# Kernel optimization log

Hardware: AMD Instinct MI355X
Metric: run time of the kernel (lower is better)

The kernel has to match this reference:

```python
import jax, jax.numpy as jnp
import numpy as np

B, S, H, NH, E, F = 4, 1024, 1024, 16, 8, 4096
D = H // NH  # head_dim = 64
EPS = 1e-5


def _layernorm(x, g, b):
    mu = jnp.mean(x, axis=-1, keepdims=True)
    var = jnp.var(x, axis=-1, keepdims=True)
    return (x - mu) * jax.lax.rsqrt(var + EPS) * g + b


def setup_inputs() -> dict:
    key = jax.random.key(0)
    ks = jax.random.split(key, 16)
    s = 0.02
    return {
        "x": jax.random.normal(ks[0], (B, S, H), jnp.float32),
        "ln1_g": jnp.ones((H,), jnp.float32),
        "ln1_b": jnp.zeros((H,), jnp.float32),
        "ln2_g": jnp.ones((H,), jnp.float32),
        "ln2_b": jnp.zeros((H,), jnp.float32),
        "wq": jax.random.normal(ks[1], (H, H), jnp.float32) * s,
        "bq": jnp.zeros((H,), jnp.float32),
        "wk": jax.random.normal(ks[2], (H, H), jnp.float32) * s,
        "bk": jnp.zeros((H,), jnp.float32),
        "wv": jax.random.normal(ks[3], (H, H), jnp.float32) * s,
        "bv": jnp.zeros((H,), jnp.float32),
        "wo": jax.random.normal(ks[4], (H, H), jnp.float32) * s,
        "bo": jnp.zeros((H,), jnp.float32),
        "gate_w": jax.random.normal(ks[5], (H, E), jnp.float32) * s,
        "gate_b": jnp.zeros((E,), jnp.float32),
        "w1": jax.random.normal(ks[6], (E, H, F), jnp.float32) * s,
        "b1": jnp.zeros((E, F), jnp.float32),
        "w2": jax.random.normal(ks[7], (E, F, H), jnp.float32) * s,
        "b2": jnp.zeros((E, H), jnp.float32),
    }


def reference(x, ln1_g, ln1_b, ln2_g, ln2_b, wq, bq, wk, bk, wv, bv, wo, bo,
              gate_w, gate_b, w1, b1, w2, b2):
    b, s, h = x.shape
    # ---- attention sub-layer ----
    hn = _layernorm(x, ln1_g, ln1_b)
    q = (hn @ wq + bq).reshape(b, s, NH, D).transpose(0, 2, 1, 3)  # [B,NH,S,D]
    k = (hn @ wk + bk).reshape(b, s, NH, D).transpose(0, 2, 1, 3)
    v = (hn @ wv + bv).reshape(b, s, NH, D).transpose(0, 2, 1, 3)
    scores = jnp.einsum('bhqd,bhkd->bhqk', q, k) / jnp.sqrt(jnp.float32(D))
    attn = jax.nn.softmax(scores, axis=-1)
    o = jnp.einsum('bhqk,bhkd->bhqd', attn, v)
    o = o.transpose(0, 2, 1, 3).reshape(b, s, h)
    x = x + (o @ wo + bo)
    # ---- MoE sub-layer (top-1 routing; output NOT scaled by gate prob) ----
    hn2 = _layernorm(x, ln2_g, ln2_b).reshape(-1, h)  # [T,H]
    logits = hn2 @ gate_w + gate_b                    # [T,E]
    idx = jnp.argmax(logits, axis=-1)                 # argmax(softmax)=argmax(logits)
    # dense compute of all experts, then top-1 select (jit-friendly dispatch)
    mid = jax.nn.relu(jnp.einsum('th,ehf->etf', hn2, w1) + b1[:, None, :])  # [E,T,F]
    y = jnp.einsum('etf,efh->eth', mid, w2) + b2[:, None, :]                # [E,T,H]
    moe = y[idx, jnp.arange(hn2.shape[0])]            # [T,H]
    return x + moe.reshape(b, s, h)
```

## Files before the change

### kernel.cpp

```cpp
#include <hip/hip_runtime.h>
#include <math.h>


constexpr int NB = 4, NS = 1024, NHID = 1024, NHEAD = 16, HD = 64, NE = 8, NF = 4096;
constexpr int NT = NB * NS;
constexpr float LN_EPS = 1e-5f;
constexpr size_t MiB = 1048576;

using bf16x8 = __attribute__((ext_vector_type(8))) short;
using f32x4  = __attribute__((ext_vector_type(4))) float;
using f32x16 = __attribute__((ext_vector_type(16))) float;
using u32x2  = __attribute__((ext_vector_type(2))) unsigned int;

__device__ __forceinline__ unsigned short f2bf(float x) {
    unsigned u = __float_as_uint(x);
    return (unsigned short)((u + 0x7fffu + ((u >> 16) & 1u)) >> 16);
}
__device__ __forceinline__ float bf2f(unsigned short h) {
    return __uint_as_float((unsigned)h << 16);
}

__device__ __forceinline__ void gload_lds16(const void* g, void* l) {
    __builtin_amdgcn_global_load_lds(
        (const __attribute__((address_space(1))) void*)g,
        (__attribute__((address_space(3))) void*)l, 16, 0, 0);
}

template<int MODE>
__global__ __launch_bounds__(256)
void ln_kernel(const float* __restrict__ x, const float* __restrict__ g,
               const float* __restrict__ b, float* __restrict__ y,
               unsigned short* __restrict__ yh, unsigned short* __restrict__ yl)
{
    const int t = blockIdx.x, tid = threadIdx.x;
    const float4 xv = ((const float4*)(x + (size_t)t * NHID))[tid];
    float s  = xv.x + xv.y + xv.z + xv.w;
    float sq = xv.x*xv.x + xv.y*xv.y + xv.z*xv.z + xv.w*xv.w;
    for (int off = 32; off > 0; off >>= 1) {
        s  += __shfl_down(s, off);
        sq += __shfl_down(sq, off);
    }
    __shared__ float ws_[4], wsq_[4], stats[2];
    const int wid = tid >> 6, lane = tid & 63;
    if (lane == 0) { ws_[wid] = s; wsq_[wid] = sq; }
    __syncthreads();
    if (tid == 0) {
        const float ts = ws_[0] + ws_[1] + ws_[2] + ws_[3];
        const float tq = wsq_[0] + wsq_[1] + wsq_[2] + wsq_[3];
        const float mu = ts * (1.0f / NHID);
        const float var = tq * (1.0f / NHID) - mu * mu;
        stats[0] = mu; stats[1] = rsqrtf(var + LN_EPS);
    }
    __syncthreads();
    const float mu = stats[0], rs = stats[1];
    const float4 gv = ((const float4*)g)[tid];
    const float4 bv = ((const float4*)b)[tid];
    float ov[4];
    ov[0] = (xv.x - mu) * rs * gv.x + bv.x;
    ov[1] = (xv.y - mu) * rs * gv.y + bv.y;
    ov[2] = (xv.z - mu) * rs * gv.z + bv.z;
    ov[3] = (xv.w - mu) * rs * gv.w + bv.w;
    if (MODE == 1) {
        float4 o4; o4.x = ov[0]; o4.y = ov[1]; o4.z = ov[2]; o4.w = ov[3];
        ((float4*)(y + (size_t)t * NHID))[tid] = o4;
    }
    unsigned long long ph = 0, pl = 0;
    #pragma unroll
    for (int j = 0; j < 4; ++j) {
        const unsigned short h = f2bf(ov[j]);
        ph |= (unsigned long long)h << (16 * j);
        if (MODE == 0) pl |= (unsigned long long)f2bf(ov[j] - bf2f(h)) << (16 * j);
    }
    ((unsigned long long*)(yh + (size_t)t * NHID))[tid] = ph;
    if (MODE == 0)
        ((unsigned long long*)(yl + (size_t)t * NHID))[tid] = pl;
}

__global__ __launch_bounds__(256)
void pack_whl(const float* __restrict__ w, unsigned short* __restrict__ out,
              int K, int N)
{
    const int k8 = blockIdx.y;
    const int col = blockIdx.x * 256 + threadIdx.x;
    const float* src = w + (size_t)k8 * 8 * N + col;
    unsigned short th[8] __attribute__((aligned(16)));
    unsigned short tl[8] __attribute__((aligned(16)));
    #pragma unroll
    for (int j = 0; j < 8; ++j) {
        const float f = src[(size_t)j * N];
        th[j] = f2bf(f);
        tl[j] = f2bf(f - bf2f(th[j]));
    }
    const size_t plane = (size_t)(K / 8) * N * 8;
    const size_t o = ((size_t)k8 * N + col) * 8;
    *(f32x4*)(out + o)         = *(const f32x4*)th;
    *(f32x4*)(out + plane + o) = *(const f32x4*)tl;
}

__global__ __launch_bounds__(256)
void pack_w(const float* __restrict__ w, unsigned short* __restrict__ out,
            int K, int N)
{
    const int e = blockIdx.z, k8 = blockIdx.y;
    const int col = blockIdx.x * 256 + threadIdx.x;
    const float* src = w + ((size_t)e * K + (size_t)k8 * 8) * N + col;
    unsigned short tmp[8] __attribute__((aligned(16)));
    #pragma unroll
    for (int j = 0; j < 8; ++j) tmp[j] = f2bf(src[(size_t)j * N]);
    *(f32x4*)(out + (((size_t)e * (K / 8) + k8) * N + col) * 8) = *(const f32x4*)tmp;
}

template<bool QKV3, bool RESID>
__global__ __launch_bounds__(256, 2)
void gemm3(const unsigned short* __restrict__ Ah, const unsigned short* __restrict__ Al,
           const unsigned short* __restrict__ Bp,
           const float* __restrict__ b0, const float* __restrict__ b1,
           const float* __restrict__ b2,
           const float* __restrict__ resid, float* __restrict__ C,
           int N, int K)
{
    __shared__ __attribute__((aligned(16))) unsigned short Ahs[4 * 128 * 8];
    __shared__ __attribute__((aligned(16))) unsigned short Als[4 * 128 * 8];
    __shared__ __attribute__((aligned(16))) unsigned short Bhs[4 * 128 * 8];
    __shared__ __attribute__((aligned(16))) unsigned short Bls[4 * 128 * 8];

    const int z  = QKV3 ? blockIdx.z : 0;
    const int m0 = blockIdx.y * 128;
    const int n0 = blockIdx.x * 128;
    const size_t plane = (size_t)(K / 8) * N * 8;
    const unsigned short* Bh = Bp + (size_t)z * 2 * plane;
    const unsigned short* Bl = Bh + plane;
    const float* bp = QKV3 ? (z == 0 ? b0 : z == 1 ? b1 : b2) : b0;
    float* Cp = C + (QKV3 ? (size_t)z * NT * N : 0);

    const int tid  = threadIdx.x;
    const int lane = tid & 63, wid = tid >> 6;
    const int quad = lane >> 4, l16 = lane & 15;
    const int wm = (wid >> 1) * 64;
    const int wn = (wid & 1) * 64;

    const unsigned short *gAh[2], *gAl[2], *gBh[2], *gBl[2];
    void *lAh[2], *lAl[2], *lBh[2], *lBl[2];
    #pragma unroll
    for (int i = 0; i < 2; ++i) {
        const int c = tid + 256 * i;
        const int q = c >> 7, idx = c & 127;
        gAh[i] = Ah + (size_t)(m0 + idx) * K + q * 8;
        gAl[i] = Al + (size_t)(m0 + idx) * K + q * 8;
        gBh[i] = Bh + ((size_t)q * N + n0 + idx) * 8;
        gBl[i] = Bl + ((size_t)q * N + n0 + idx) * 8;
        lAh[i] = (void*)&Ahs[(size_t)c * 8];
        lAl[i] = (void*)&Als[(size_t)c * 8];
        lBh[i] = (void*)&Bhs[(size_t)c * 8];
        lBl[i] = (void*)&Bls[(size_t)c * 8];
    }

    f32x4 acc[4][4];
    #pragma unroll
    for (int mi = 0; mi < 4; ++mi)
        #pragma unroll
        for (int ni = 0; ni < 4; ++ni)
            acc[mi][ni] = (f32x4){0.f, 0.f, 0.f, 0.f};

    const size_t bstep = (size_t)4 * N * 8;
    for (int ks = 0; ks < K / 32; ++ks) {
        __syncthreads();
        #pragma unroll
        for (int i = 0; i < 2; ++i) {
            gload_lds16(gAh[i], lAh[i]);
            gload_lds16(gAl[i], lAl[i]);
            gload_lds16(gBh[i], lBh[i]);
            gload_lds16(gBl[i], lBl[i]);
            gAh[i] += 32; gAl[i] += 32; gBh[i] += bstep; gBl[i] += bstep;
        }
        __syncthreads();

        bf16x8 ah[4], al[4], bh[4], bl[4];
        #pragma unroll
        for (int mi = 0; mi < 4; ++mi) {
            ah[mi] = *(const bf16x8*)&Ahs[((size_t)quad * 128 + wm + mi * 16 + l16) * 8];
            al[mi] = *(const bf16x8*)&Als[((size_t)quad * 128 + wm + mi * 16 + l16) * 8];
        }
        #pragma unroll
        for (int ni = 0; ni < 4; ++ni) {
            bh[ni] = *(const bf16x8*)&Bhs[((size_t)quad * 128 + wn + ni * 16 + l16) * 8];
            bl[ni] = *(const bf16x8*)&Bls[((size_t)quad * 128 + wn + ni * 16 + l16) * 8];
        }
        #pragma unroll
        for (int mi = 0; mi < 4; ++mi)
            #pragma unroll
            for (int ni = 0; ni < 4; ++ni) {
                acc[mi][ni] = __builtin_amdgcn_mfma_f32_16x16x32_bf16(
                    ah[mi], bh[ni], acc[mi][ni], 0, 0, 0);
                acc[mi][ni] = __builtin_amdgcn_mfma_f32_16x16x32_bf16(
                    ah[mi], bl[ni], acc[mi][ni], 0, 0, 0);
                acc[mi][ni] = __builtin_amdgcn_mfma_f32_16x16x32_bf16(
                    al[mi], bh[ni], acc[mi][ni], 0, 0, 0);
            }
    }

    #pragma unroll
    for (int mi = 0; mi < 4; ++mi) {
        const int rbase = wm + mi * 16 + quad * 4;
        #pragma unroll
        for (int r = 0; r < 4; ++r) {
            const size_t gm = m0 + rbase + r;
            #pragma unroll
            for (int ni = 0; ni < 4; ++ni) {
                const int col = n0 + wn + ni * 16 + l16;
                float vv = acc[mi][ni][r] + bp[col];
                if (RESID) vv += resid[gm * N + col];
                Cp[gm * N + col] = vv;
            }
        }
    }
}

__global__ __launch_bounds__(256, 2)
void attn_kernel(const float* __restrict__ q, const float* __restrict__ k,
                 const float* __restrict__ v,
                 unsigned short* __restrict__ oh, unsigned short* __restrict__ ol)
{
    struct KV {
        unsigned short Kp[2][4160];
        unsigned short Vp[2][4096];
    };
    __shared__ union SMem { KV kv; float O[4 * 64 * 33]; } sm;
    __shared__ float linv[128];

    const int qt = blockIdx.x, hh = blockIdx.y, b = blockIdx.z;
    const int tid = threadIdx.x;
    const int lane = tid & 63, w = tid >> 6;
    const int l31 = lane & 31, hf = lane >> 5;

    const size_t rowbase = (size_t)b * NS;
    const size_t cb = (size_t)hh * HD;

    float4 kreg[4], vreg[2][2];
    auto loadKV = [&](int kt) {
        #pragma unroll
        for (int i = 0; i < 4; ++i) {
            const int c = tid + 256 * i, j = c >> 4, d4 = (c & 15) << 2;
            kreg[i] = *(const float4*)(k + (rowbase + kt * 64 + j) * NHID + cb + d4);
        }
        #pragma unroll
        for (int i = 0; i < 2; ++i) {
            const int c = tid + 256 * i;
            const int j2 = ((c >> 6) << 3) + (((c >> 4) & 3) << 1);
            const int d4 = (c & 15) << 2;
            vreg[i][0] = *(const float4*)(v + (rowbase + kt * 64 + j2) * NHID + cb + d4);
            vreg[i][1] = *(const float4*)(v + (rowbase + kt * 64 + j2 + 1) * NHID + cb + d4);
        }
    };
    loadKV(0);

    bf16x8 qfh[4], qfl[4];
    {
        const int qrow = qt * 128 + w * 32 + l31;
        const float* qp = q + (rowbase + qrow) * NHID + cb + hf * 8;
        #pragma unroll
        for (int s = 0; s < 4; ++s) {
            const float4 f0 = *(const float4*)(qp + s * 16);
            const float4 f1 = *(const float4*)(qp + s * 16 + 4);
            const float ff[8] = {f0.x, f0.y, f0.z, f0.w, f1.x, f1.y, f1.z, f1.w};
            #pragma unroll
            for (int e = 0; e < 8; ++e) {
                const float sv = ff[e] * 0.125f;
                const unsigned short hv = f2bf(sv);
                qfh[s][e] = (short)hv;
                qfl[s][e] = (short)f2bf(sv - bf2f(hv));
            }
        }
    }

    f32x16 oa[2];
    #pragma unroll
    for (int mfd = 0; mfd < 2; ++mfd)
        #pragma unroll
        for (int r = 0; r < 16; ++r) oa[mfd][r] = 0.f;
    float m_run = -1e30f, l_run = 0.f;

    for (int kt = 0; kt < NS / 64; ++kt) {
        __syncthreads();

        #pragma unroll
        for (int i = 0; i < 4; ++i) {
            const int c = tid + 256 * i, j = c >> 4, d4 = (c & 15) << 2;
            const float* f = (const float*)&kreg[i];
            unsigned short hs[4], ls[4];
            #pragma unroll
            for (int e = 0; e < 4; ++e) {
                hs[e] = f2bf(f[e]); ls[e] = f2bf(f[e] - bf2f(hs[e]));
            }
            u32x2 wh, wl;
            wh[0] = hs[0] | ((unsigned)hs[1] << 16); wh[1] = hs[2] | ((unsigned)hs[3] << 16);
            wl[0] = ls[0] | ((unsigned)ls[1] << 16); wl[1] = ls[2] | ((unsigned)ls[3] << 16);
            const int ad = (d4 >> 3) * 520 + j * 8 + (d4 & 7);
            *(u32x2*)&sm.kv.Kp[0][ad] = wh;
            *(u32x2*)&sm.kv.Kp[1][ad] = wl;
        }
        #pragma unroll
        for (int i = 0; i < 2; ++i) {
            const int c = tid + 256 * i;
            const int j2 = ((c >> 6) << 3) + (((c >> 4) & 3) << 1);
            const int d4 = (c & 15) << 2;
            const float* fa = (const float*)&vreg[i][0];
            const float* fb = (const float*)&vreg[i][1];
            #pragma unroll
            for (int dd = 0; dd < 4; ++dd) {
                const int d = d4 + dd;
                const unsigned short ah_ = f2bf(fa[dd]), bh_ = f2bf(fb[dd]);
                const unsigned short al_ = f2bf(fa[dd] - bf2f(ah_));
                const unsigned short bl_ = f2bf(fb[dd] - bf2f(bh_));
                const int ad = d * 64 + (((j2 >> 3) ^ (d & 7)) << 3) + (j2 & 7);
                *(unsigned*)&sm.kv.Vp[0][ad] = ah_ | ((unsigned)bh_ << 16);
                *(unsigned*)&sm.kv.Vp[1][ad] = al_ | ((unsigned)bl_ << 16);
            }
        }
        if (kt + 1 < NS / 64) loadKV(kt + 1);
        __syncthreads();

        f32x16 sa[2];
        #pragma unroll
        for (int mf = 0; mf < 2; ++mf)
            #pragma unroll
            for (int r = 0; r < 16; ++r) sa[mf][r] = 0.f;
        #pragma unroll
        for (int mf = 0; mf < 2; ++mf) {
            bf16x8 kf[4];
            #pragma unroll
            for (int s = 0; s < 4; ++s)
                kf[s] = *(const bf16x8*)&sm.kv.Kp[0][(2*s+hf)*520 + (mf*32+l31)*8];
            #pragma unroll
            for (int s = 0; s < 4; ++s)
                sa[mf] = __builtin_amdgcn_mfma_f32_32x32x16_bf16(kf[s], qfh[s], sa[mf], 0, 0, 0);
            #pragma unroll
            for (int s = 0; s < 4; ++s)
                sa[mf] = __builtin_amdgcn_mfma_f32_32x32x16_bf16(kf[s], qfl[s], sa[mf], 0, 0, 0);
            #pragma unroll
            for (int s = 0; s < 4; ++s)
                kf[s] = *(const bf16x8*)&sm.kv.Kp[1][(2*s+hf)*520 + (mf*32+l31)*8];
            #pragma unroll
            for (int s = 0; s < 4; ++s)
                sa[mf] = __builtin_amdgcn_mfma_f32_32x32x16_bf16(kf[s], qfh[s], sa[mf], 0, 0, 0);
        }

        float tm = sa[0][0];
        #pragma unroll
        for (int r = 1; r < 16; ++r) tm = fmaxf(tm, sa[0][r]);
        #pragma unroll
        for (int r = 0; r < 16; ++r) tm = fmaxf(tm, sa[1][r]);
        tm = fmaxf(tm, __shfl_xor(tm, 32));
        const float newm = fmaxf(m_run, tm);
        const float al = __expf(m_run - newm);
        m_run = newm;
        float ps = 0.f;
        #pragma unroll
        for (int mf = 0; mf < 2; ++mf)
            #pragma unroll
            for (int r = 0; r < 16; ++r) {
                const float pv = __expf(sa[mf][r] - newm);
                sa[mf][r] = pv; ps += pv;
            }
        ps += __shfl_xor(ps, 32);
        l_run = l_run * al + ps;
        #pragma unroll
        for (int mfd = 0; mfd < 2; ++mfd)
            #pragma unroll
            for (int r = 0; r < 16; ++r) oa[mfd][r] *= al;

        bf16x8 pfh[4], pfl[4];
        #pragma unroll
        for (int t = 0; t < 4; ++t) {
            const int mfp = t >> 1, u8 = (t & 1) * 8;
            unsigned short hb[8]; float lo8[8];
            #pragma unroll
            for (int e = 0; e < 8; ++e) {
                const float pv = sa[mfp][u8 + e];
                hb[e] = f2bf(pv); lo8[e] = pv - bf2f(hb[e]);
            }
            {
                const unsigned X0 = hb[0] | ((unsigned)hb[1] << 16);
                const unsigned X1 = hb[2] | ((unsigned)hb[3] << 16);
                const unsigned X2 = hb[4] | ((unsigned)hb[5] << 16);
                const unsigned X3 = hb[6] | ((unsigned)hb[7] << 16);
                const unsigned s0 = (unsigned)__shfl_xor((int)X0, 32);
                const unsigned s1 = (unsigned)__shfl_xor((int)X1, 32);
                const unsigned s2 = (unsigned)__shfl_xor((int)X2, 32);
                const unsigned s3 = (unsigned)__shfl_xor((int)X3, 32);
                union UU { unsigned wd[4]; bf16x8 vv; } uu;
                uu.wd[0] = hf ? s2 : X0;
                uu.wd[1] = hf ? s3 : X1;
                uu.wd[2] = hf ? X2 : s0;
                uu.wd[3] = hf ? X3 : s1;
                pfh[t] = uu.vv;
            }
            {
                unsigned short lb[8];
                #pragma unroll
                for (int e = 0; e < 8; ++e) lb[e] = f2bf(lo8[e]);
                const unsigned Y0 = lb[0] | ((unsigned)lb[1] << 16);
                const unsigned Y1 = lb[2] | ((unsigned)lb[3] << 16);
                const unsigned Y2 = lb[4] | ((unsigned)lb[5] << 16);
                const unsigned Y3 = lb[6] | ((unsigned)lb[7] << 16);
                const unsigned s0 = (unsigned)__shfl_xor((int)Y0, 32);
                const unsigned s1 = (unsigned)__shfl_xor((int)Y1, 32);
                const unsigned s2 = (unsigned)__shfl_xor((int)Y2, 32);
                const unsigned s3 = (unsigned)__shfl_xor((int)Y3, 32);
                union UU { unsigned wd[4]; bf16x8 vv; } uu;
                uu.wd[0] = hf ? s2 : Y0;
                uu.wd[1] = hf ? s3 : Y1;
                uu.wd[2] = hf ? Y2 : s0;
                uu.wd[3] = hf ? Y3 : s1;
                pfl[t] = uu.vv;
            }
        }

        #pragma unroll
        for (int mfd = 0; mfd < 2; ++mfd) {
            const int db = (mfd * 32 + l31) * 64;
            const int sw = l31 & 7;
            bf16x8 vf[4];
            #pragma unroll
            for (int ks = 0; ks < 4; ++ks)
                vf[ks] = *(const bf16x8*)&sm.kv.Vp[0][db + (((2*ks+hf) ^ sw) << 3)];
            #pragma unroll
            for (int ks = 0; ks < 4; ++ks)
                oa[mfd] = __builtin_amdgcn_mfma_f32_32x32x16_bf16(vf[ks], pfh[ks], oa[mfd], 0, 0, 0);
            #pragma unroll
            for (int ks = 0; ks < 4; ++ks)
                oa[mfd] = __builtin_amdgcn_mfma_f32_32x32x16_bf16(vf[ks], pfl[ks], oa[mfd], 0, 0, 0);
            #pragma unroll
            for (int ks = 0; ks < 4; ++ks)
                vf[ks] = *(const bf16x8*)&sm.kv.Vp[1][db + (((2*ks+hf) ^ sw) << 3)];
            #pragma unroll
            for (int ks = 0; ks < 4; ++ks)
                oa[mfd] = __builtin_amdgcn_mfma_f32_32x32x16_bf16(vf[ks], pfh[ks], oa[mfd], 0, 0, 0);
        }
    }

    __syncthreads();
    {
        float* Ow = sm.O + w * (64 * 33);
        #pragma unroll
        for (int mfd = 0; mfd < 2; ++mfd)
            #pragma unroll
            for (int r = 0; r < 16; ++r) {
                const int dr = mfd * 32 + (r & 3) + 8 * (r >> 2) + 4 * hf;
                Ow[dr * 33 + l31] = oa[mfd][r];
            }
        if (hf == 0) linv[w * 32 + l31] = 1.0f / l_run;
    }
    __syncthreads();
    #pragma unroll
    for (int it = 0; it < 8; ++it) {
        const int c = tid + 256 * it;
        const int qq = c >> 4, d4 = (c & 15) << 2;
        const float* Or = sm.O + (qq >> 5) * (64 * 33) + (qq & 31);
        const float sc_ = linv[qq];
        unsigned short hs[4], ls[4];
        #pragma unroll
        for (int e = 0; e < 4; ++e) {
            const float vv = Or[(d4 + e) * 33] * sc_;
            hs[e] = f2bf(vv); ls[e] = f2bf(vv - bf2f(hs[e]));
        }
        u32x2 ph_, pl_;
        ph_[0] = hs[0] | ((unsigned)hs[1] << 16); ph_[1] = hs[2] | ((unsigned)hs[3] << 16);
        pl_[0] = ls[0] | ((unsigned)ls[1] << 16); pl_[1] = ls[2] | ((unsigned)ls[3] << 16);
        const size_t o = (rowbase + qt * 128 + qq) * NHID + cb + d4;
        *(u32x2*)&oh[o] = ph_;
        *(u32x2*)&ol[o] = pl_;
    }
}

__global__ __launch_bounds__(64)
void gate_kernel(const float* __restrict__ hn2, const float* __restrict__ gw,
                 const float* __restrict__ gb, int* __restrict__ counts,
                 int* __restrict__ tok)
{
    const int t = blockIdx.x, lane = threadIdx.x;
    const float* row = hn2 + (size_t)t * NHID;
    float acc[NE] = {};
    for (int hh = lane; hh < NHID; hh += 64) {
        const float xv = row[hh];
        const float4 g0 = ((const float4*)(gw + (size_t)hh * NE))[0];
        const float4 g1 = ((const float4*)(gw + (size_t)hh * NE))[1];
        acc[0] += xv * g0.x; acc[1] += xv * g0.y; acc[2] += xv * g0.z; acc[3] += xv * g0.w;
        acc[4] += xv * g1.x; acc[5] += xv * g1.y; acc[6] += xv * g1.z; acc[7] += xv * g1.w;
    }
    #pragma unroll
    for (int e = 0; e < NE; ++e)
        for (int off = 32; off > 0; off >>= 1)
            acc[e] += __shfl_down(acc[e], off);
    if (lane == 0) {
        float best = -1e30f; int bi = 0;
        #pragma unroll
        for (int e = 0; e < NE; ++e) {
            const float lv = acc[e] + gb[e];
            if (lv > best) { best = lv; bi = e; }
        }
        const int pos = atomicAdd(&counts[bi], 1);
        tok[(size_t)bi * NT + pos] = t;
    }
}

template<int BN, int MSPLIT, bool BF16OUT>
__global__ __launch_bounds__(256, 2)
void moe_gemm(const unsigned short* __restrict__ A,
              const unsigned short* __restrict__ Bp,
              const float* __restrict__ bias,
              const float* __restrict__ resid,
              void* __restrict__ Cout,
              int N, int K,
              const int* __restrict__ rows, const int* __restrict__ counts)
{
    constexpr int NI = BN / 32;
    constexpr int NBCH = (4 * BN) / 256;
    __shared__ __attribute__((aligned(16))) unsigned short As[2][4 * 128 * 8];
    __shared__ __attribute__((aligned(16))) unsigned short Bs[2][4 * BN * 8];

    const int id = blockIdx.x;
    const int e  = id & 7;
    const int nn = N / BN;
    const int nb = (id >> 3) % nn;
    const int r0 = (id >> 3) / nn;
    const int n0 = nb * BN;

    const int Meff = counts[e];
    const int* rl = rows + (size_t)e * NT;
    const int nmt = (Meff + 127) >> 7;

    const int tid  = threadIdx.x;
    const int lane = tid & 63, wid = tid >> 6;
    const int quad = lane >> 4, l16 = lane & 15;
    const int wm = (wid >> 1) * 64;
    const int wn = (wid & 1) * (BN / 2);
    const int NK = K / 32;
    const size_t bstep = (size_t)4 * N * 8;

    for (int mt = r0; mt < nmt; mt += MSPLIT) {
        const int m0 = mt * 128;

        const unsigned short* gA[2];
        #pragma unroll
        for (int i = 0; i < 2; ++i) {
            const int c = tid + 256 * i;
            const int q = c >> 7, row = c & 127;
            int m = m0 + row; if (m >= Meff) m = Meff - 1;
            gA[i] = A + (size_t)rl[m] * K + q * 8;
        }
        const unsigned short* gB[NBCH];
        #pragma unroll
        for (int i = 0; i < NBCH; ++i) {
            const int c = tid + 256 * i;
            const int q = c / BN, n = c % BN;
            gB[i] = Bp + (((size_t)e * (K / 8) + q) * N + n0 + n) * 8;
        }

        f32x4 acc[4][NI];
        #pragma unroll
        for (int mi = 0; mi < 4; ++mi)
            #pragma unroll
            for (int ni = 0; ni < NI; ++ni)
                acc[mi][ni] = (f32x4){0.f, 0.f, 0.f, 0.f};

        gload_lds16(gA[0], (void*)&As[0][(size_t)tid * 8]);
        gload_lds16(gA[1], (void*)&As[0][(size_t)(tid + 256) * 8]);
        #pragma unroll
        for (int i = 0; i < NBCH; ++i)
            gload_lds16(gB[i], (void*)&Bs[0][(size_t)(tid + 256 * i) * 8]);
        gA[0] += 32; gA[1] += 32;
        #pragma unroll
        for (int i = 0; i < NBCH; ++i) gB[i] += bstep;
        __syncthreads();

        for (int ks = 0; ks < NK; ++ks) {
            const int cur = ks & 1, nxt = cur ^ 1;
            if (ks + 1 < NK) {
                gload_lds16(gA[0], (void*)&As[nxt][(size_t)tid * 8]);
                gload_lds16(gA[1], (void*)&As[nxt][(size_t)(tid + 256) * 8]);
                #pragma unroll
                for (int i = 0; i < NBCH; ++i)
                    gload_lds16(gB[i], (void*)&Bs[nxt][(size_t)(tid + 256 * i) * 8]);
                gA[0] += 32; gA[1] += 32;
                #pragma unroll
                for (int i = 0; i < NBCH; ++i) gB[i] += bstep;
            }

            bf16x8 af[4], bfr[NI];
            #pragma unroll
            for (int mi = 0; mi < 4; ++mi)
                af[mi] = *(const bf16x8*)&As[cur][((size_t)quad * 128 + wm + mi * 16 + l16) * 8];
            #pragma unroll
            for (int ni = 0; ni < NI; ++ni)
                bfr[ni] = *(const bf16x8*)&Bs[cur][((size_t)quad * BN + wn + ni * 16 + l16) * 8];
            #pragma unroll
            for (int mi = 0; mi < 4; ++mi)
                #pragma unroll
                for (int ni = 0; ni < NI; ++ni)
                    acc[mi][ni] = __builtin_amdgcn_mfma_f32_16x16x32_bf16(
                        af[mi], bfr[ni], acc[mi][ni], 0, 0, 0);
            __syncthreads();
        }

        #pragma unroll
        for (int mi = 0; mi < 4; ++mi) {
            const int rbase = wm + mi * 16 + quad * 4;
            #pragma unroll
            for (int r = 0; r < 4; ++r) {
                const int m = m0 + rbase + r;
                if (m >= Meff) continue;
                const int gr = rl[m];
                #pragma unroll
                for (int ni = 0; ni < NI; ++ni) {
                    const int col = n0 + wn + ni * 16 + l16;
                    float vv = acc[mi][ni][r] + bias[(size_t)e * N + col];
                    if (BF16OUT) {
                        vv = fmaxf(vv, 0.f);
                        ((unsigned short*)Cout)[(size_t)gr * N + col] = f2bf(vv);
                    } else {
                        vv += resid[(size_t)gr * N + col];
                        ((float*)Cout)[(size_t)gr * N + col] = vv;
                    }
                }
            }
        }
    }
}

extern "C" void kernel_launch(void* const* d_in, const int* in_sizes, int n_in,
                              void* d_out, int out_size, void* d_ws, size_t ws_size,
                              hipStream_t stream)
{
    (void)in_sizes; (void)n_in; (void)out_size; (void)ws_size;
    const float* x      = (const float*)d_in[0];
    const float* ln1_g  = (const float*)d_in[1];
    const float* ln1_b  = (const float*)d_in[2];
    const float* ln2_g  = (const float*)d_in[3];
    const float* ln2_b  = (const float*)d_in[4];
    const float* wq     = (const float*)d_in[5];
    const float* bq     = (const float*)d_in[6];
    const float* wk     = (const float*)d_in[7];
    const float* bk     = (const float*)d_in[8];
    const float* wv     = (const float*)d_in[9];
    const float* bv     = (const float*)d_in[10];
    const float* wo     = (const float*)d_in[11];
    const float* bo     = (const float*)d_in[12];
    const float* gate_w = (const float*)d_in[13];
    const float* gate_b = (const float*)d_in[14];
    const float* w1     = (const float*)d_in[15];
    const float* b1     = (const float*)d_in[16];
    const float* w2     = (const float*)d_in[17];
    const float* b2     = (const float*)d_in[18];
    float* out = (float*)d_out;

    char* W8 = (char*)d_ws;
    float*          qbuf   = (float*)(W8);
    float*          kbuf   = (float*)(W8 + 16 * MiB);
    float*          vbuf   = (float*)(W8 + 32 * MiB);
    unsigned short* hnh    = (unsigned short*)(W8 + 48 * MiB);
    unsigned short* hnl    = (unsigned short*)(W8 + 56 * MiB);
    unsigned short* ohb    = (unsigned short*)(W8 + 48 * MiB);
    unsigned short* olb    = (unsigned short*)(W8 + 56 * MiB);
    unsigned short* qkvpk  = (unsigned short*)(W8 + 64 * MiB);
    unsigned short* wopk   = (unsigned short*)(W8 + 76 * MiB);
    unsigned short* hn2bf  = (unsigned short*)(W8 + 64 * MiB);
    int*            tok    = (int*)(W8 + 72 * MiB);
    int*            cnts   = (int*)(W8 + 72 * MiB + (size_t)NE * NT * 4);
    float*          x2buf  = (float*)(W8 + 80 * MiB);
    float*          hn2f   = (float*)(W8 + 96 * MiB);
    unsigned short* mid    = (unsigned short*)(W8 + 96 * MiB);
    unsigned short* wpack  = (unsigned short*)(W8);

    const size_t wsz = (size_t)2 * NHID * NHID;

    {
        dim3 g(NHID / 256, NHID / 8, 1);
        pack_whl<<<g, 256, 0, stream>>>(wq, qkvpk,           NHID, NHID);
        pack_whl<<<g, 256, 0, stream>>>(wk, qkvpk + wsz,     NHID, NHID);
        pack_whl<<<g, 256, 0, stream>>>(wv, qkvpk + 2 * wsz, NHID, NHID);
        pack_whl<<<g, 256, 0, stream>>>(wo, wopk,            NHID, NHID);
    }

    ln_kernel<0><<<NT, 256, 0, stream>>>(x, ln1_g, ln1_b, nullptr, hnh, hnl);

    {
        dim3 g(NHID / 128, NT / 128, 3);
        gemm3<true, false><<<g, 256, 0, stream>>>(
            hnh, hnl, qkvpk, bq, bk, bv, nullptr, qbuf, NHID, NHID);
    }

    {
        dim3 g(NS / 128, NHEAD, NB);
        attn_kernel<<<g, 256, 0, stream>>>(qbuf, kbuf, vbuf, ohb, olb);
    }

    {
        dim3 g(NHID / 128, NT / 128, 1);
        gemm3<false, true><<<g, 256, 0, stream>>>(
            ohb, olb, wopk, bo, nullptr, nullptr, x, x2buf, NHID, NHID);
    }

    ln_kernel<1><<<NT, 256, 0, stream>>>(x2buf, ln2_g, ln2_b, hn2f, hn2bf, nullptr);

    hipMemsetAsync(cnts, 0, NE * sizeof(int), stream);
    gate_kernel<<<NT, 64, 0, stream>>>(hn2f, gate_w, gate_b, cnts, tok);

    {
        dim3 g(NF / 256, NHID / 8, NE);
        pack_w<<<g, 256, 0, stream>>>(w1, wpack, NHID, NF);
    }
    moe_gemm<128, 2, true><<<NE * (NF / 128) * 2, 256, 0, stream>>>(
        hn2bf, wpack, b1, nullptr, mid, NF, NHID, tok, cnts);
    {
        dim3 g(NHID / 256, NF / 8, NE);
        pack_w<<<g, 256, 0, stream>>>(w2, wpack, NF, NHID);
    }
    moe_gemm<64, 4, false><<<NE * (NHID / 64) * 4, 256, 0, stream>>>(
        mid, wpack, b2, x2buf, out, NHID, NF, tok, cnts);
}
```

Baseline: 922.6 us.

## Triple-buffer MoE GEMM LDS pipeline with vmcnt waits and raise occupancy

After: 839.7 us. 9.0% less time.

```diff
diff --git a/kernel.cpp b/kernel.cpp
--- a/kernel.cpp
+++ b/kernel.cpp
@@ -505,7 +505,7 @@
 }
 
 template<int BN, int MSPLIT, bool BF16OUT>
-__global__ __launch_bounds__(256, 2)
+__global__ __launch_bounds__(256, 4)
 void moe_gemm(const unsigned short* __restrict__ A,
               const unsigned short* __restrict__ Bp,
               const float* __restrict__ bias,
@@ -516,8 +516,9 @@
 {
     constexpr int NI = BN / 32;
     constexpr int NBCH = (4 * BN) / 256;
-    __shared__ __attribute__((aligned(16))) unsigned short As[2][4 * 128 * 8];
-    __shared__ __attribute__((aligned(16))) unsigned short Bs[2][4 * BN * 8];
+    constexpr int W = 2 + NBCH;
+    __shared__ __attribute__((aligned(16))) unsigned short As[3][4 * 128 * 8];
+    __shared__ __attribute__((aligned(16))) unsigned short Bs[3][4 * BN * 8];
 
     const int id = blockIdx.x;
     const int e  = id & 7;
@@ -540,6 +541,7 @@
 
     for (int mt = r0; mt < nmt; mt += MSPLIT) {
         const int m0 = mt * 128;
+        __syncthreads();
 
         const unsigned short* gA[2];
         #pragma unroll
@@ -557,6 +559,17 @@
             gB[i] = Bp + (((size_t)e * (K / 8) + q) * N + n0 + n) * 8;
         }
 
+        auto stage = [&](int b) {
+            gload_lds16(gA[0], (void*)&As[b][(size_t)tid * 8]);
+            gload_lds16(gA[1], (void*)&As[b][(size_t)(tid + 256) * 8]);
+            #pragma unroll
+            for (int i = 0; i < NBCH; ++i)
+                gload_lds16(gB[i], (void*)&Bs[b][(size_t)(tid + 256 * i) * 8]);
+            gA[0] += 32; gA[1] += 32;
+            #pragma unroll
+            for (int i = 0; i < NBCH; ++i) gB[i] += bstep;
+        };
+
         f32x4 acc[4][NI];
         #pragma unroll
         for (int mi = 0; mi < 4; ++mi)
@@ -564,27 +577,21 @@
             for (int ni = 0; ni < NI; ++ni)
                 acc[mi][ni] = (f32x4){0.f, 0.f, 0.f, 0.f};
 
-        gload_lds16(gA[0], (void*)&As[0][(size_t)tid * 8]);
-        gload_lds16(gA[1], (void*)&As[0][(size_t)(tid + 256) * 8]);
-        #pragma unroll
-        for (int i = 0; i < NBCH; ++i)
-            gload_lds16(gB[i], (void*)&Bs[0][(size_t)(tid + 256 * i) * 8]);
-        gA[0] += 32; gA[1] += 32;
-        #pragma unroll
-        for (int i = 0; i < NBCH; ++i) gB[i] += bstep;
-        __syncthreads();
-
+        stage(0);
+        stage(1);
+
+        int cur = 0;
         for (int ks = 0; ks < NK; ++ks) {
-            const int cur = ks & 1, nxt = cur ^ 1;
-            if (ks + 1 < NK) {
-                gload_lds16(gA[0], (void*)&As[nxt][(size_t)tid * 8]);
-                gload_lds16(gA[1], (void*)&As[nxt][(size_t)(tid + 256) * 8]);
-                #pragma unroll
-                for (int i = 0; i < NBCH; ++i)
-                    gload_lds16(gB[i], (void*)&Bs[nxt][(size_t)(tid + 256 * i) * 8]);
-                gA[0] += 32; gA[1] += 32;
-                #pragma unroll
-                for (int i = 0; i < NBCH; ++i) gB[i] += bstep;
+            if (ks < NK - 1)
+                asm volatile("s_waitcnt vmcnt(%0)" :: "n"(W) : "memory");
+            else
+                asm volatile("s_waitcnt vmcnt(0)" ::: "memory");
+            __builtin_amdgcn_s_barrier();
+            asm volatile("" ::: "memory");
+
+            if (ks + 2 < NK) {
+                const int nx = cur >= 1 ? cur - 1 : cur + 2;
+                stage(nx);
             }
 
             bf16x8 af[4], bfr[NI];
@@ -600,7 +607,8 @@
                 for (int ni = 0; ni < NI; ++ni)
                     acc[mi][ni] = __builtin_amdgcn_mfma_f32_16x16x32_bf16(
                         af[mi], bfr[ni], acc[mi][ni], 0, 0, 0);
-            __syncthreads();
+
+            cur = cur == 2 ? 0 : cur + 1;
         }
 
         #pragma unroll
@@ -710,12 +718,12 @@
         dim3 g(NF / 256, NHID / 8, NE);
         pack_w<<<g, 256, 0, stream>>>(w1, wpack, NHID, NF);
     }
-    moe_gemm<128, 2, true><<<NE * (NF / 128) * 2, 256, 0, stream>>>(
+    moe_gemm<128, 3, true><<<NE * (NF / 128) * 3, 256, 0, stream>>>(
         hn2bf, wpack, b1, nullptr, mid, NF, NHID, tok, cnts);
     {
         dim3 g(NHID / 256, NF / 8, NE);
         pack_w<<<g, 256, 0, stream>>>(w2, wpack, NF, NHID);
     }
-    moe_gemm<64, 4, false><<<NE * (NHID / 64) * 4, 256, 0, stream>>>(
+    moe_gemm<64, 5, false><<<NE * (NHID / 64) * 5, 256, 0, stream>>>(
         mid, wpack, b2, x2buf, out, NHID, NF, tok, cnts);
 }
```
